# Optimization experiments

Hardware: AMD Instinct MI355X
Metric: run time of the kernel (lower is better)

## Reference

```python
import jax, jax.numpy as jnp
import numpy as np

D_K = 64
SCALE = jnp.sqrt(jnp.float32(D_K))

def setup_inputs() -> dict:
    key = jax.random.key(0)
    kq, kk, kv = jax.random.split(key, 3)
    shape = (2, 16, 2048, D_K)  # [batch, heads, seq, d_k]
    return {
        "Q": jax.random.normal(kq, shape, dtype=jnp.float32),
        "K": jax.random.normal(kk, shape, dtype=jnp.float32),
        "V": jax.random.normal(kv, shape, dtype=jnp.float32),
    }

def reference(Q, K, V):
    # scores: [B, H, S, S]
    scores = jnp.einsum("bhqd,bhkd->bhqk", Q, K) / SCALE
    weights = jax.nn.softmax(scores, axis=-1)
    return jnp.einsum("bhqk,bhkd->bhqd", weights, V)
```

## Files before the change

kernel.cpp:

```cpp
#include <hip/hip_runtime.h>
#include <math.h>

#define S_LEN 2048
#define DK 64
#define BH 32
#define BQ 128
#define BK 64
#define NT 32
#define TILE_US 8192
#define TILE_B  16384

#if defined(__has_builtin)
#if __has_builtin(__builtin_amdgcn_exp2f)
#define EXP2F(x) __builtin_amdgcn_exp2f(x)
#else
#define EXP2F(x) exp2f(x)
#endif
#else
#define EXP2F(x) exp2f(x)
#endif

typedef _Float16 f16x8 __attribute__((ext_vector_type(8)));
typedef __fp16   fp16x2 __attribute__((ext_vector_type(2)));
typedef float    f32x16 __attribute__((ext_vector_type(16)));

#define MFMAH(a,b,c) __builtin_amdgcn_mfma_f32_32x32x16_f16((a),(b),(c),0,0,0)

union U16H { uint4 u; f16x8 h; unsigned short s[8]; };

__device__ __forceinline__ f16x8 ldsh8(const unsigned short* p){
    U16H t; t.u = *(const uint4*)p; return t.h;
}
__device__ __forceinline__ f16x8 u4h(unsigned a, unsigned b, unsigned c, unsigned d){
    U16H t; t.u = make_uint4(a,b,c,d); return t.h;
}
__device__ __forceinline__ unsigned pk16(float a, float b){
    union { fp16x2 h; unsigned u; } c;
    c.h = __builtin_amdgcn_cvt_pkrtz(a, b);
    return c.u;
}
__device__ __forceinline__ unsigned short f16b(float x){
    union { _Float16 f; unsigned short s; } c; c.f = (_Float16)x; return c.s;
}
__device__ __forceinline__ void gl_lds16(const void* g, void* l){
    __builtin_amdgcn_global_load_lds(
        (const __attribute__((address_space(1))) void*)g,
        (__attribute__((address_space(3))) void*)l, 16, 0, 0);
}

__global__ __launch_bounds__(256) void prep(const float* __restrict__ K,
                                            const float* __restrict__ V,
                                            unsigned short* __restrict__ W) {
    __shared__ unsigned short Vt[64 * 72];
    const int t = threadIdx.x;
    const int head = blockIdx.x >> 5;
    const int kb = blockIdx.x & 31;
    const size_t hbase = (size_t)head * S_LEN * DK;
    unsigned short* Wt = W + (size_t)(head * NT + kb) * TILE_US;

    {
        const int row = t >> 2;
        const int c0 = (t & 3) * 16;
        const float* vp = V + hbase + (size_t)(kb * BK + row) * DK + c0;
        #pragma unroll
        for (int i = 0; i < 4; ++i) {
            const float4 q = *(const float4*)(vp + 4 * i);
            const int c = c0 + 4 * i;
            Vt[(c + 0) * 72 + row] = f16b(q.x);
            Vt[(c + 1) * 72 + row] = f16b(q.y);
            Vt[(c + 2) * 72 + row] = f16b(q.z);
            Vt[(c + 3) * 72 + row] = f16b(q.w);
        }
    }
    #pragma unroll
    for (int i = 0; i < 2; ++i) {
        const int P = i * 256 + t;
        const int r = P >> 3, p = P & 7;
        const int ch = p ^ (r & 7);
        const float* kp = K + hbase + (size_t)(kb * BK + r) * DK + ch * 8;
        const float4 a = *(const float4*)kp;
        const float4 b = *(const float4*)(kp + 4);
        *(uint4*)(Wt + P * 8) = make_uint4(pk16(a.x, a.y), pk16(a.z, a.w),
                                           pk16(b.x, b.y), pk16(b.z, b.w));
    }
    __syncthreads();
    #pragma unroll
    for (int i = 0; i < 2; ++i) {
        const int P = i * 256 + t;
        const int d = P >> 3, p = P & 7;
        const int ch = p ^ (d & 7);
        const uint4 u = *(const uint4*)(Vt + d * 72 + ch * 8);
        *(uint4*)(Wt + 4096 + P * 8) = u;
    }
}

__global__ __launch_bounds__(256) void fa3(const float* __restrict__ Q,
                                           const unsigned short* __restrict__ W,
                                           float* __restrict__ O) {
    __shared__ __align__(16) unsigned short SB[2 * TILE_US];

    const int tid = threadIdx.x;
    const int wq  = tid >> 6;
    const int lane = tid & 63;
    const int L31 = tid & 31;
    const int q5  = (tid >> 5) & 1;
    const int swz = L31 & 7;

    const int bid  = blockIdx.x;
    const int x    = bid & 7, g = bid >> 3;
    const int head = ((g >> 4) << 3) | x;
    const int qb   = g & 15;
    const size_t hbase = (size_t)head * S_LEN * DK;
    const unsigned short* Wh = W + (size_t)head * NT * TILE_US;

    const float c1 = 0.18033688011112042f;
    f16x8 qf[4];
    {
        const int qrow = qb * BQ + wq * 32 + L31;
        const float* qp = Q + hbase + (size_t)qrow * DK;
        #pragma unroll
        for (int ks = 0; ks < 4; ++ks) {
            const float4 a = *(const float4*)(qp + ks * 16 + q5 * 8);
            const float4 b = *(const float4*)(qp + ks * 16 + q5 * 8 + 4);
            qf[ks] = u4h(pk16(a.x * c1, a.y * c1), pk16(a.z * c1, a.w * c1),
                         pk16(b.x * c1, b.y * c1), pk16(b.z * c1, b.w * c1));
        }
    }

    {
        const char* src = (const char*)Wh + wq * 4096 + lane * 16;
        char* dst = (char*)SB + wq * 4096;
        #pragma unroll
        for (int j = 0; j < 4; ++j) gl_lds16(src + j * 1024, dst + j * 1024);
    }
    __syncthreads();

    f32x16 accO0 = {}, accO1 = {};
    float l0 = 0.f;

    for (int kb = 0; kb < NT; ++kb) {
        const int cur = kb & 1;
        if (kb + 1 < NT) {
            const char* src = (const char*)Wh + (size_t)(kb + 1) * TILE_B + wq * 4096 + lane * 16;
            char* dst = (char*)SB + (cur ^ 1) * TILE_B + wq * 4096;
            #pragma unroll
            for (int j = 0; j < 4; ++j) gl_lds16(src + j * 1024, dst + j * 1024);
        }
        const unsigned short* B0 = SB + cur * TILE_US;

        f32x16 s0 = {}, s1 = {};
        #pragma unroll
        for (int ks = 0; ks < 4; ++ks) {
            const int ch = ((ks * 2 + q5) ^ swz) * 8;
            const unsigned short* pk_ = B0 + L31 * 64 + ch;
            const f16x8 a0 = ldsh8(pk_);
            const f16x8 a1 = ldsh8(pk_ + 2048);
            s0 = MFMAH(a0, qf[ks], s0);
            s1 = MFMAH(a1, qf[ks], s1);
        }

        float rs = 0.f;
        #pragma unroll
        for (int r = 0; r < 16; ++r) {
            s0[r] = EXP2F(s0[r]); rs += s0[r];
            s1[r] = EXP2F(s1[r]); rs += s1[r];
        }
        rs += __shfl_xor(rs, 32);
        l0 += rs;

        unsigned P2[2][4][2];
        #pragma unroll
        for (int b = 0; b < 4; ++b) {
            P2[0][b][0] = pk16(s0[4*b+0], s0[4*b+1]);
            P2[0][b][1] = pk16(s0[4*b+2], s0[4*b+3]);
            P2[1][b][0] = pk16(s1[4*b+0], s1[4*b+1]);
            P2[1][b][1] = pk16(s1[4*b+2], s1[4*b+3]);
        }

        #pragma unroll
        for (int ks = 0; ks < 4; ++ks) {
            const int mt = ks >> 1, kk2 = (ks & 1) * 2;
            const unsigned own0 = q5 ? P2[mt][kk2+1][0] : P2[mt][kk2][0];
            const unsigned own1 = q5 ? P2[mt][kk2+1][1] : P2[mt][kk2][1];
            const unsigned snd0 = q5 ? P2[mt][kk2][0]   : P2[mt][kk2+1][0];
            const unsigned snd1 = q5 ? P2[mt][kk2][1]   : P2[mt][kk2+1][1];
            const unsigned r0 = (unsigned)__shfl_xor((int)snd0, 32);
            const unsigned r1 = (unsigned)__shfl_xor((int)snd1, 32);
            const f16x8 ph = q5 ? u4h(r0, r1, own0, own1) : u4h(own0, own1, r0, r1);

            const int ch = ((ks * 2 + q5) ^ swz) * 8;
            const unsigned short* pv = B0 + 4096 + L31 * 64 + ch;
            const f16x8 v0 = ldsh8(pv);
            const f16x8 v1 = ldsh8(pv + 2048);
            accO0 = MFMAH(v0, ph, accO0);
            accO1 = MFMAH(v1, ph, accO1);
        }
        __syncthreads();
    }

    const float inv = 1.f / l0;
    const int qrow = qb * BQ + wq * 32 + L31;
    float* op = O + hbase + (size_t)qrow * DK;
    #pragma unroll
    for (int b = 0; b < 4; ++b) {
        float4 o0;
        o0.x = accO0[4*b+0] * inv; o0.y = accO0[4*b+1] * inv;
        o0.z = accO0[4*b+2] * inv; o0.w = accO0[4*b+3] * inv;
        *(float4*)(op + 8 * b + 4 * q5) = o0;
        float4 o1;
        o1.x = accO1[4*b+0] * inv; o1.y = accO1[4*b+1] * inv;
        o1.z = accO1[4*b+2] * inv; o1.w = accO1[4*b+3] * inv;
        *(float4*)(op + 32 + 8 * b + 4 * q5) = o1;
    }
}

extern "C" void kernel_launch(void* const* d_in, const int* in_sizes, int n_in,
                              void* d_out, int out_size, void* d_ws, size_t ws_size,
                              hipStream_t stream) {
    const float* Q = (const float*)d_in[0];
    const float* K = (const float*)d_in[1];
    const float* V = (const float*)d_in[2];
    float* O = (float*)d_out;
    unsigned short* W = (unsigned short*)d_ws;
    prep<<<dim3(BH * NT), dim3(256), 0, stream>>>(K, V, W);
    fa3<<<dim3(512), dim3(256), 0, stream>>>(Q, W, O);
}
```

Before: 146.4 us.

## Split key range across two wave groups per block and merge partials in LDS

Doubles the block to 512 threads. Each half processes half of the key/value tiles with its own double-buffered LDS region, then the halves combine their unnormalized outputs and row sums through shared memory before the final normalization. This aims to raise waves per CU and shorten the serial key loop. It costs a doubled LDS footprint, a merge step, and block-wide barriers that now span eight waves.

```diff
diff --git a/kernel.cpp b/kernel.cpp
--- a/kernel.cpp
+++ b/kernel.cpp
@@ -7,6 +7,7 @@
 #define BQ 128
 #define BK 64
 #define NT 32
+#define NTH 16
 #define TILE_US 8192
 #define TILE_B  16384
 
@@ -94,13 +95,15 @@
     }
 }
 
-__global__ __launch_bounds__(256) void fa3(const float* __restrict__ Q,
+__global__ __launch_bounds__(512) void fa4(const float* __restrict__ Q,
                                            const unsigned short* __restrict__ W,
                                            float* __restrict__ O) {
-    __shared__ __align__(16) unsigned short SB[2 * TILE_US];
+    __shared__ __align__(16) unsigned short SB[4 * TILE_US];
+    __shared__ float Lbuf[BQ];
 
     const int tid = threadIdx.x;
-    const int wq  = tid >> 6;
+    const int kh  = tid >> 8;
+    const int wq  = (tid >> 6) & 3;
     const int lane = tid & 63;
     const int L31 = tid & 31;
     const int q5  = (tid >> 5) & 1;
@@ -112,6 +115,7 @@
     const int qb   = g & 15;
     const size_t hbase = (size_t)head * S_LEN * DK;
     const unsigned short* Wh = W + (size_t)head * NT * TILE_US;
+    unsigned short* SBh = SB + kh * 2 * TILE_US;
 
     const float c1 = 0.18033688011112042f;
     f16x8 qf[4];
@@ -128,8 +132,8 @@
     }
 
     {
-        const char* src = (const char*)Wh + wq * 4096 + lane * 16;
-        char* dst = (char*)SB + wq * 4096;
+        const char* src = (const char*)Wh + (size_t)(kh * NTH) * TILE_B + wq * 4096 + lane * 16;
+        char* dst = (char*)SBh + wq * 4096;
         #pragma unroll
         for (int j = 0; j < 4; ++j) gl_lds16(src + j * 1024, dst + j * 1024);
     }
@@ -138,15 +142,15 @@
     f32x16 accO0 = {}, accO1 = {};
     float l0 = 0.f;
 
-    for (int kb = 0; kb < NT; ++kb) {
-        const int cur = kb & 1;
-        if (kb + 1 < NT) {
-            const char* src = (const char*)Wh + (size_t)(kb + 1) * TILE_B + wq * 4096 + lane * 16;
-            char* dst = (char*)SB + (cur ^ 1) * TILE_B + wq * 4096;
+    for (int it = 0; it < NTH; ++it) {
+        const int cur = it & 1;
+        if (it + 1 < NTH) {
+            const char* src = (const char*)Wh + (size_t)(kh * NTH + it + 1) * TILE_B + wq * 4096 + lane * 16;
+            char* dst = (char*)SBh + (cur ^ 1) * TILE_B + wq * 4096;
             #pragma unroll
             for (int j = 0; j < 4; ++j) gl_lds16(src + j * 1024, dst + j * 1024);
         }
-        const unsigned short* B0 = SB + cur * TILE_US;
+        const unsigned short* B0 = SBh + cur * TILE_US;
 
         f32x16 s0 = {}, s1 = {};
         #pragma unroll
@@ -198,19 +202,38 @@
         __syncthreads();
     }
 
-    const float inv = 1.f / l0;
-    const int qrow = qb * BQ + wq * 32 + L31;
-    float* op = O + hbase + (size_t)qrow * DK;
-    #pragma unroll
-    for (int b = 0; b < 4; ++b) {
-        float4 o0;
-        o0.x = accO0[4*b+0] * inv; o0.y = accO0[4*b+1] * inv;
-        o0.z = accO0[4*b+2] * inv; o0.w = accO0[4*b+3] * inv;
-        *(float4*)(op + 8 * b + 4 * q5) = o0;
-        float4 o1;
-        o1.x = accO1[4*b+0] * inv; o1.y = accO1[4*b+1] * inv;
-        o1.z = accO1[4*b+2] * inv; o1.w = accO1[4*b+3] * inv;
-        *(float4*)(op + 32 + 8 * b + 4 * q5) = o1;
+    float* Mbuf = (float*)SB;
+    const int q = wq * 32 + L31;
+    if (kh == 1) {
+        float* mp = Mbuf + q * 68;
+        #pragma unroll
+        for (int b = 0; b < 4; ++b) {
+            *(float4*)(mp + 8 * b + 4 * q5) =
+                make_float4(accO0[4*b+0], accO0[4*b+1], accO0[4*b+2], accO0[4*b+3]);
+            *(float4*)(mp + 32 + 8 * b + 4 * q5) =
+                make_float4(accO1[4*b+0], accO1[4*b+1], accO1[4*b+2], accO1[4*b+3]);
+        }
+        if (q5 == 0) Lbuf[q] = l0;
+    }
+    __syncthreads();
+    if (kh == 0) {
+        const float inv = 1.f / (l0 + Lbuf[q]);
+        const float* mp = Mbuf + q * 68;
+        const int qrow = qb * BQ + q;
+        float* op = O + hbase + (size_t)qrow * DK;
+        #pragma unroll
+        for (int b = 0; b < 4; ++b) {
+            const float4 m0 = *(const float4*)(mp + 8 * b + 4 * q5);
+            float4 o0;
+            o0.x = (accO0[4*b+0] + m0.x) * inv; o0.y = (accO0[4*b+1] + m0.y) * inv;
+            o0.z = (accO0[4*b+2] + m0.z) * inv; o0.w = (accO0[4*b+3] + m0.w) * inv;
+            *(float4*)(op + 8 * b + 4 * q5) = o0;
+            const float4 m1 = *(const float4*)(mp + 32 + 8 * b + 4 * q5);
+            float4 o1;
+            o1.x = (accO1[4*b+0] + m1.x) * inv; o1.y = (accO1[4*b+1] + m1.y) * inv;
+            o1.z = (accO1[4*b+2] + m1.z) * inv; o1.w = (accO1[4*b+3] + m1.w) * inv;
+            *(float4*)(op + 32 + 8 * b + 4 * q5) = o1;
+        }
     }
 }
 
@@ -223,5 +246,5 @@
     float* O = (float*)d_out;
     unsigned short* W = (unsigned short*)d_ws;
     prep<<<dim3(BH * NT), dim3(256), 0, stream>>>(K, V, W);
-    fa3<<<dim3(512), dim3(256), 0, stream>>>(Q, W, O);
-}
+    fa4<<<dim3(512), dim3(512), 0, stream>>>(Q, W, O);
+}
```

New measurement: 138.0 us. 1.06x faster.

## Pre-swizzle K/V into MFMA fragment order and load directly to registers

Applied to the files above, without the earlier changes.

The prep kernel now writes K and V tiles in the exact per-lane MFMA operand order, so the attention kernel can read each fragment with coalesced 16-byte global loads straight into registers. This drops the LDS staging, double buffering and block-wide barriers. The attention kernel becomes one 64-thread wave per 32-row query strip on 2048 blocks, and the row-sum shuffle is deferred to the end. The trade-off is that every wave rereads K/V through L2 with no sharing across waves in LDS, and global load latency is no longer hidden by an explicit prefetch.

```diff
diff --git a/kernel.cpp b/kernel.cpp
--- a/kernel.cpp
+++ b/kernel.cpp
@@ -4,7 +4,6 @@
 #define S_LEN 2048
 #define DK 64
 #define BH 32
-#define BQ 128
 #define BK 64
 #define NT 32
 #define TILE_US 8192
@@ -28,9 +27,7 @@
 
 union U16H { uint4 u; f16x8 h; unsigned short s[8]; };
 
-__device__ __forceinline__ f16x8 ldsh8(const unsigned short* p){
-    U16H t; t.u = *(const uint4*)p; return t.h;
-}
+__device__ __forceinline__ f16x8 asf16(uint4 u){ U16H t; t.u = u; return t.h; }
 __device__ __forceinline__ f16x8 u4h(unsigned a, unsigned b, unsigned c, unsigned d){
     U16H t; t.u = make_uint4(a,b,c,d); return t.h;
 }
@@ -42,81 +39,58 @@
 __device__ __forceinline__ unsigned short f16b(float x){
     union { _Float16 f; unsigned short s; } c; c.f = (_Float16)x; return c.s;
 }
-__device__ __forceinline__ void gl_lds16(const void* g, void* l){
-    __builtin_amdgcn_global_load_lds(
-        (const __attribute__((address_space(1))) void*)g,
-        (__attribute__((address_space(3))) void*)l, 16, 0, 0);
-}
 
-__global__ __launch_bounds__(256) void prep(const float* __restrict__ K,
-                                            const float* __restrict__ V,
-                                            unsigned short* __restrict__ W) {
-    __shared__ unsigned short Vt[64 * 72];
+__global__ __launch_bounds__(256) void prep2(const float* __restrict__ K,
+                                             const float* __restrict__ V,
+                                             unsigned short* __restrict__ W) {
     const int t = threadIdx.x;
     const int head = blockIdx.x >> 5;
     const int kb = blockIdx.x & 31;
-    const size_t hbase = (size_t)head * S_LEN * DK;
+    const size_t tbase = (size_t)head * S_LEN * DK + (size_t)kb * BK * DK;
     unsigned short* Wt = W + (size_t)(head * NT + kb) * TILE_US;
 
-    {
-        const int row = t >> 2;
-        const int c0 = (t & 3) * 16;
-        const float* vp = V + hbase + (size_t)(kb * BK + row) * DK + c0;
-        #pragma unroll
-        for (int i = 0; i < 4; ++i) {
-            const float4 q = *(const float4*)(vp + 4 * i);
-            const int c = c0 + 4 * i;
-            Vt[(c + 0) * 72 + row] = f16b(q.x);
-            Vt[(c + 1) * 72 + row] = f16b(q.y);
-            Vt[(c + 2) * 72 + row] = f16b(q.z);
-            Vt[(c + 3) * 72 + row] = f16b(q.w);
-        }
-    }
     #pragma unroll
     for (int i = 0; i < 2; ++i) {
         const int P = i * 256 + t;
-        const int r = P >> 3, p = P & 7;
-        const int ch = p ^ (r & 7);
-        const float* kp = K + hbase + (size_t)(kb * BK + r) * DK + ch * 8;
+        const int ks = P >> 7, rhi = (P >> 6) & 1, q5 = (P >> 5) & 1, r31 = P & 31;
+        const float* kp = K + tbase + (size_t)(rhi * 32 + r31) * DK + ks * 16 + q5 * 8;
         const float4 a = *(const float4*)kp;
         const float4 b = *(const float4*)(kp + 4);
         *(uint4*)(Wt + P * 8) = make_uint4(pk16(a.x, a.y), pk16(a.z, a.w),
                                            pk16(b.x, b.y), pk16(b.z, b.w));
     }
-    __syncthreads();
     #pragma unroll
     for (int i = 0; i < 2; ++i) {
         const int P = i * 256 + t;
-        const int d = P >> 3, p = P & 7;
-        const int ch = p ^ (d & 7);
-        const uint4 u = *(const uint4*)(Vt + d * 72 + ch * 8);
-        *(uint4*)(Wt + 4096 + P * 8) = u;
+        const int ks = P >> 7, dhi = (P >> 6) & 1, q5 = (P >> 5) & 1, d31 = P & 31;
+        const int d = dhi * 32 + d31;
+        const float* vp = V + tbase + (size_t)(ks * 16 + q5 * 8) * DK + d;
+        U16H o;
+        #pragma unroll
+        for (int j = 0; j < 8; ++j) o.s[j] = f16b(vp[(size_t)j * DK]);
+        *(uint4*)(Wt + 4096 + P * 8) = o.u;
     }
 }
 
-__global__ __launch_bounds__(256) void fa3(const float* __restrict__ Q,
-                                           const unsigned short* __restrict__ W,
-                                           float* __restrict__ O) {
-    __shared__ __align__(16) unsigned short SB[2 * TILE_US];
-
-    const int tid = threadIdx.x;
-    const int wq  = tid >> 6;
-    const int lane = tid & 63;
-    const int L31 = tid & 31;
-    const int q5  = (tid >> 5) & 1;
-    const int swz = L31 & 7;
+__global__ __launch_bounds__(64) void fa5(const float* __restrict__ Q,
+                                          const unsigned short* __restrict__ W,
+                                          float* __restrict__ O) {
+    const int lane = threadIdx.x;
+    const int L31 = lane & 31;
+    const int q5  = lane >> 5;
 
     const int bid  = blockIdx.x;
     const int x    = bid & 7, g = bid >> 3;
-    const int head = ((g >> 4) << 3) | x;
-    const int qb   = g & 15;
+    const int head = ((g >> 6) << 3) | x;
+    const int strip = g & 63;
     const size_t hbase = (size_t)head * S_LEN * DK;
-    const unsigned short* Wh = W + (size_t)head * NT * TILE_US;
+    const unsigned short* Wk = W + (size_t)head * NT * TILE_US;
+    const unsigned short* Wv = Wk + 4096;
 
     const float c1 = 0.18033688011112042f;
     f16x8 qf[4];
     {
-        const int qrow = qb * BQ + wq * 32 + L31;
+        const int qrow = strip * 32 + L31;
         const float* qp = Q + hbase + (size_t)qrow * DK;
         #pragma unroll
         for (int ks = 0; ks < 4; ++ks) {
@@ -127,46 +101,39 @@
         }
     }
 
-    {
-        const char* src = (const char*)Wh + wq * 4096 + lane * 16;
-        char* dst = (char*)SB + wq * 4096;
-        #pragma unroll
-        for (int j = 0; j < 4; ++j) gl_lds16(src + j * 1024, dst + j * 1024);
-    }
-    __syncthreads();
-
     f32x16 accO0 = {}, accO1 = {};
-    float l0 = 0.f;
+    float lsum = 0.f;
 
     for (int kb = 0; kb < NT; ++kb) {
-        const int cur = kb & 1;
-        if (kb + 1 < NT) {
-            const char* src = (const char*)Wh + (size_t)(kb + 1) * TILE_B + wq * 4096 + lane * 16;
-            char* dst = (char*)SB + (cur ^ 1) * TILE_B + wq * 4096;
-            #pragma unroll
-            for (int j = 0; j < 4; ++j) gl_lds16(src + j * 1024, dst + j * 1024);
+        const unsigned short* Kt = Wk + (size_t)kb * TILE_US;
+        const unsigned short* Vt = Wv + (size_t)kb * TILE_US;
+
+        uint4 ka0[4], ka1[4];
+        #pragma unroll
+        for (int ks = 0; ks < 4; ++ks) {
+            ka0[ks] = *(const uint4*)(Kt + ks * 1024 + lane * 8);
+            ka1[ks] = *(const uint4*)(Kt + ks * 1024 + 512 + lane * 8);
         }
-        const unsigned short* B0 = SB + cur * TILE_US;
 
         f32x16 s0 = {}, s1 = {};
         #pragma unroll
         for (int ks = 0; ks < 4; ++ks) {
-            const int ch = ((ks * 2 + q5) ^ swz) * 8;
-            const unsigned short* pk_ = B0 + L31 * 64 + ch;
-            const f16x8 a0 = ldsh8(pk_);
-            const f16x8 a1 = ldsh8(pk_ + 2048);
-            s0 = MFMAH(a0, qf[ks], s0);
-            s1 = MFMAH(a1, qf[ks], s1);
+            s0 = MFMAH(asf16(ka0[ks]), qf[ks], s0);
+            s1 = MFMAH(asf16(ka1[ks]), qf[ks], s1);
         }
 
-        float rs = 0.f;
+        uint4 va0[4], va1[4];
+        #pragma unroll
+        for (int ks = 0; ks < 4; ++ks) {
+            va0[ks] = *(const uint4*)(Vt + ks * 1024 + lane * 8);
+            va1[ks] = *(const uint4*)(Vt + ks * 1024 + 512 + lane * 8);
+        }
+
         #pragma unroll
         for (int r = 0; r < 16; ++r) {
-            s0[r] = EXP2F(s0[r]); rs += s0[r];
-            s1[r] = EXP2F(s1[r]); rs += s1[r];
+            s0[r] = EXP2F(s0[r]); lsum += s0[r];
+            s1[r] = EXP2F(s1[r]); lsum += s1[r];
         }
-        rs += __shfl_xor(rs, 32);
-        l0 += rs;
 
         unsigned P2[2][4][2];
         #pragma unroll
@@ -188,18 +155,14 @@
             const unsigned r1 = (unsigned)__shfl_xor((int)snd1, 32);
             const f16x8 ph = q5 ? u4h(r0, r1, own0, own1) : u4h(own0, own1, r0, r1);
 
-            const int ch = ((ks * 2 + q5) ^ swz) * 8;
-            const unsigned short* pv = B0 + 4096 + L31 * 64 + ch;
-            const f16x8 v0 = ldsh8(pv);
-            const f16x8 v1 = ldsh8(pv + 2048);
-            accO0 = MFMAH(v0, ph, accO0);
-            accO1 = MFMAH(v1, ph, accO1);
+            accO0 = MFMAH(asf16(va0[ks]), ph, accO0);
+            accO1 = MFMAH(asf16(va1[ks]), ph, accO1);
         }
-        __syncthreads();
     }
 
-    const float inv = 1.f / l0;
-    const int qrow = qb * BQ + wq * 32 + L31;
+    const float l = lsum + __shfl_xor(lsum, 32);
+    const float inv = 1.f / l;
+    const int qrow = strip * 32 + L31;
     float* op = O + hbase + (size_t)qrow * DK;
     #pragma unroll
     for (int b = 0; b < 4; ++b) {
@@ -222,6 +185,6 @@
     const float* V = (const float*)d_in[2];
     float* O = (float*)d_out;
     unsigned short* W = (unsigned short*)d_ws;
-    prep<<<dim3(BH * NT), dim3(256), 0, stream>>>(K, V, W);
-    fa3<<<dim3(512), dim3(256), 0, stream>>>(Q, W, O);
+    prep2<<<dim3(BH * NT), dim3(256), 0, stream>>>(K, V, W);
+    fa5<<<dim3(2048), dim3(64), 0, stream>>>(Q, W, O);
 }
```

Measured after the change: 144.3 us. No clear change (-1.4%).
